# Performance work log

Hardware: AMD Instinct MI355X
Metric: run time of the kernel (lower is better)

## Reference

```python
import jax, jax.numpy as jnp
import numpy as np

N = 1_000_000
D1 = 16          # n_input_1 (first-layer features, cols 0:16)
D2 = 16          # n_input_2 (second-layer features, cols 16:32)
NC = 64          # n_clusters (first layer)
NCPC = 8         # n_clusters_per_cluster (second layer)


def setup_inputs() -> dict:
    key = jax.random.key(0)
    k1, k2, k3 = jax.random.split(key, 3)
    x = jax.random.normal(k1, (N, D1 + D2), dtype=jnp.float32)
    centers_outer = jax.random.normal(k2, (NC, D1), dtype=jnp.float32)
    centers_inner = jax.random.normal(k3, (NC, NCPC, D2), dtype=jnp.float32)
    return {"x": x, "centers_outer": centers_outer, "centers_inner": centers_inner}


def reference(x, centers_outer, centers_inner):
    # x: [N, D1+D2]; input_1_idx = cols [0:D1], input_2_idx = cols [D1:D1+D2]
    x1 = x[:, :D1]
    x2 = x[:, D1:]

    # First-layer nearest-centroid assignment (squared Euclidean).
    # ||x1 - c||^2 = ||x1||^2 - 2 x1.c + ||c||^2; the ||x1||^2 term is
    # constant over clusters so it does not affect the argmin.
    d1 = jnp.sum(centers_outer ** 2, axis=-1)[None, :] - 2.0 * (x1 @ centers_outer.T)  # [N, NC]
    outer = jnp.argmin(d1, axis=1)  # [N] int

    # Second-layer assignment: each sample only compares against the NCPC
    # sub-centers of its outer cluster (this fuses the original per-cluster
    # torch.where gather/scatter loop into one vectorized pass).
    sub = centers_inner[outer]  # [N, NCPC, D2] gather
    d2 = jnp.sum(sub ** 2, axis=-1) - 2.0 * jnp.einsum("nd,nkd->nk", x2, sub)  # [N, NCPC]
    inner = jnp.argmin(d2, axis=1)  # [N]

    return inner + outer * NCPC  # combined cluster id in [0, NC*NCPC)
```

## Files before the change

kernel.cpp:

```cpp
#include <hip/hip_runtime.h>

constexpr int D = 16;
constexpr int NC = 64;
constexpr int NCPC = 8;
constexpr int OSTRIDE = NCPC * D + 4;
constexpr int NPT = 2;
constexpr int BLOCK = 512;

__global__ __launch_bounds__(BLOCK, 2)
void cluster_kernel(const float* __restrict__ x,
                    const float* __restrict__ co,
                    const float* __restrict__ ci,
                    int* __restrict__ out, int n)
{
    __shared__ __align__(16) float s_ci[NC * OSTRIDE];
    __shared__ float s_inorm[NC * 9];

    const int t = threadIdx.x;

    const float4* ci4 = (const float4*)ci;
    #pragma unroll
    for (int i = 0; i < (NC * NCPC * D / 4) / BLOCK; ++i) {
        int idx = t + i * BLOCK;
        int o = idx >> 5;
        int f = idx & 31;
        float4 v = ci4[idx];
        *(float4*)&s_ci[o * OSTRIDE + f * 4] = v;
    }
    for (int i = t; i < NC * NCPC; i += BLOCK) {
        const float* src = ci + i * D;
        float s = 0.f;
        #pragma unroll
        for (int k = 0; k < D; ++k) s = fmaf(src[k], src[k], s);
        s_inorm[(i >> 3) * 9 + (i & 7)] = s;
    }
    float my_norm;
    {
        const float* c = co + (t & 63) * D;
        float s = 0.f;
        #pragma unroll
        for (int k = 0; k < D; ++k) s = fmaf(c[k], c[k], s);
        my_norm = s;
    }
    __syncthreads();

    const int base = blockIdx.x * (BLOCK * NPT) + t;
    #pragma unroll 1
    for (int it = 0; it < NPT; ++it) {
        int p = base + it * BLOCK;
        if (p < n) {
            const float4* xp = (const float4*)(x + (size_t)p * 32);
            float4 xa = xp[0], xb = xp[1], xc = xp[2], xd = xp[3];
            float x1[16] = {xa.x,xa.y,xa.z,xa.w, xb.x,xb.y,xb.z,xb.w,
                            xc.x,xc.y,xc.z,xc.w, xd.x,xd.y,xd.z,xd.w};

            float bestd = 3.4e38f;
            int bo = 0;
            #pragma unroll
            for (int j = 0; j < NC; ++j) {
                const float* c = co + j * D;
                float dot = 0.f;
                #pragma unroll
                for (int k = 0; k < D; ++k) dot = fmaf(x1[k], c[k], dot);
                float nj = __int_as_float(
                    __builtin_amdgcn_readlane(__float_as_int(my_norm), j));
                float d = fmaf(-2.f, dot, nj);
                if (d < bestd) { bestd = d; bo = j; }
            }

            float4 ya = xp[4], yb = xp[5], yc = xp[6], yd = xp[7];
            float x2[16] = {ya.x,ya.y,ya.z,ya.w, yb.x,yb.y,yb.z,yb.w,
                            yc.x,yc.y,yc.z,yc.w, yd.x,yd.y,yd.z,yd.w};

            const float* cb = s_ci + bo * OSTRIDE;
            const float* nb = s_inorm + bo * 9;
            float bestd2 = 3.4e38f;
            int bk = 0;
            #pragma unroll
            for (int k = 0; k < NCPC; ++k) {
                float4 c0 = *(const float4*)&cb[k * D + 0];
                float4 c1 = *(const float4*)&cb[k * D + 4];
                float4 c2 = *(const float4*)&cb[k * D + 8];
                float4 c3 = *(const float4*)&cb[k * D + 12];
                float dot = 0.f;
                dot = fmaf(x2[0],  c0.x, dot); dot = fmaf(x2[1],  c0.y, dot);
                dot = fmaf(x2[2],  c0.z, dot); dot = fmaf(x2[3],  c0.w, dot);
                dot = fmaf(x2[4],  c1.x, dot); dot = fmaf(x2[5],  c1.y, dot);
                dot = fmaf(x2[6],  c1.z, dot); dot = fmaf(x2[7],  c1.w, dot);
                dot = fmaf(x2[8],  c2.x, dot); dot = fmaf(x2[9],  c2.y, dot);
                dot = fmaf(x2[10], c2.z, dot); dot = fmaf(x2[11], c2.w, dot);
                dot = fmaf(x2[12], c3.x, dot); dot = fmaf(x2[13], c3.y, dot);
                dot = fmaf(x2[14], c3.z, dot); dot = fmaf(x2[15], c3.w, dot);
                float d = fmaf(-2.f, dot, nb[k]);
                if (d < bestd2) { bestd2 = d; bk = k; }
            }

            out[p] = bo * NCPC + bk;
        }
    }
}

extern "C" void kernel_launch(void* const* d_in, const int* in_sizes, int n_in,
                              void* d_out, int out_size, void* d_ws, size_t ws_size,
                              hipStream_t stream) {
    const float* x  = (const float*)d_in[0];
    const float* co = (const float*)d_in[1];
    const float* ci = (const float*)d_in[2];
    int* out = (int*)d_out;
    int n = in_sizes[0] / 32;
    int blocks = (n + BLOCK * NPT - 1) / (BLOCK * NPT);
    cluster_kernel<<<blocks, BLOCK, 0, stream>>>(x, co, ci, out, n);
}
```

Baseline: 198.0 us.

## Compute first-layer distances with bf16x3 split MFMA instead of scalar FMAs

The 64-centroid first-layer distance computation moves from per-thread scalar FMA loops to 32x32x16 bf16 MFMA instructions. Each fp32 operand is split into three bf16 pieces and six cross-product MFMAs are issued to keep near-fp32 accuracy. The centroid norms are folded into the accumulator init, and the argmin is reduced across the MFMA output layout and lane halves with a tie-break on the lower index. Block size and points per thread are retuned. The second-layer pass stays scalar. Rare argmin mismatches are possible from the extra rounding.

After: 191.9 us. 1.03x faster.

```diff
diff --git a/kernel.cpp b/kernel.cpp
--- a/kernel.cpp
+++ b/kernel.cpp
@@ -4,10 +4,22 @@
 constexpr int NC = 64;
 constexpr int NCPC = 8;
 constexpr int OSTRIDE = NCPC * D + 4;
-constexpr int NPT = 2;
-constexpr int BLOCK = 512;
+constexpr int BLOCK = 256;
+constexpr int NPT = 4;
 
-__global__ __launch_bounds__(BLOCK, 2)
+typedef __attribute__((ext_vector_type(8)))  short short8;
+typedef __attribute__((ext_vector_type(16))) float f32x16;
+
+static __device__ __forceinline__ unsigned f2bf(float f) {
+    unsigned u = __float_as_uint(f);
+    u += 0x7FFFu + ((u >> 16) & 1u);
+    return u >> 16;
+}
+static __device__ __forceinline__ float bf2f(unsigned h) {
+    return __uint_as_float(h << 16);
+}
+
+__global__ __launch_bounds__(BLOCK, 4)
 void cluster_kernel(const float* __restrict__ x,
                     const float* __restrict__ co,
                     const float* __restrict__ ci,
@@ -16,87 +28,160 @@
     __shared__ __align__(16) float s_ci[NC * OSTRIDE];
     __shared__ float s_inorm[NC * 9];
 
-    const int t = threadIdx.x;
+    const int t    = threadIdx.x;
+    const int lane = t & 63;
+    const int wave = t >> 6;
 
     const float4* ci4 = (const float4*)ci;
     #pragma unroll
-    for (int i = 0; i < (NC * NCPC * D / 4) / BLOCK; ++i) {
+    for (int i = 0; i < 8; ++i) {
         int idx = t + i * BLOCK;
-        int o = idx >> 5;
-        int f = idx & 31;
+        int o = idx >> 5, f = idx & 31;
         float4 v = ci4[idx];
         *(float4*)&s_ci[o * OSTRIDE + f * 4] = v;
     }
-    for (int i = t; i < NC * NCPC; i += BLOCK) {
+    #pragma unroll
+    for (int ii = 0; ii < 2; ++ii) {
+        int i = t + ii * BLOCK;
         const float* src = ci + i * D;
         float s = 0.f;
         #pragma unroll
         for (int k = 0; k < D; ++k) s = fmaf(src[k], src[k], s);
         s_inorm[(i >> 3) * 9 + (i & 7)] = s;
     }
+
     float my_norm;
     {
-        const float* c = co + (t & 63) * D;
+        const float* c = co + lane * D;
         float s = 0.f;
         #pragma unroll
         for (int k = 0; k < D; ++k) s = fmaf(c[k], c[k], s);
         my_norm = s;
     }
+
+    const int hi  = lane >> 5;
+    const int ks  = hi * 8;
+    const int hi4 = hi * 4;
+
+    float n_init[2][16];
+    #pragma unroll
+    for (int tc = 0; tc < 2; ++tc) {
+        #pragma unroll
+        for (int r = 0; r < 16; ++r) {
+            int c = tc * 32 + (r & 3) + 8 * (r >> 2) + hi4;
+            n_init[tc][r] = __int_as_float(
+                __builtin_amdgcn_ds_bpermute(c << 2, __float_as_int(my_norm)));
+        }
+    }
+
+    short8 a_h[2], a_m[2], a_l[2];
+    #pragma unroll
+    for (int tc = 0; tc < 2; ++tc) {
+        const float* cp = co + (tc * 32 + (lane & 31)) * D + ks;
+        float4 v0 = *(const float4*)cp;
+        float4 v1 = *(const float4*)(cp + 4);
+        float vv[8] = {v0.x,v0.y,v0.z,v0.w, v1.x,v1.y,v1.z,v1.w};
+        #pragma unroll
+        for (int j = 0; j < 8; ++j) {
+            float v = vv[j];
+            unsigned h = f2bf(v); float r1 = v - bf2f(h);
+            unsigned m = f2bf(r1); r1 = r1 - bf2f(m);
+            unsigned l2 = f2bf(r1);
+            a_h[tc][j] = (short)h; a_m[tc][j] = (short)m; a_l[tc][j] = (short)l2;
+        }
+    }
     __syncthreads();
 
-    const int base = blockIdx.x * (BLOCK * NPT) + t;
+    const int blockStart = blockIdx.x * (BLOCK * NPT);
     #pragma unroll 1
     for (int it = 0; it < NPT; ++it) {
-        int p = base + it * BLOCK;
-        if (p < n) {
-            const float4* xp = (const float4*)(x + (size_t)p * 32);
-            float4 xa = xp[0], xb = xp[1], xc = xp[2], xd = xp[3];
-            float x1[16] = {xa.x,xa.y,xa.z,xa.w, xb.x,xb.y,xb.z,xb.w,
-                            xc.x,xc.y,xc.z,xc.w, xd.x,xd.y,xd.z,xd.w};
+        const int S = blockStart + it * BLOCK + wave * 64;
 
-            float bestd = 3.4e38f;
-            int bo = 0;
+        int bo0 = 0, bo1 = 0;
+        #pragma unroll
+        for (int pt = 0; pt < 2; ++pt) {
+            int P = S + pt * 32 + (lane & 31);
+            P = P < n ? P : n - 1;
+            const float* xp = x + (size_t)P * 32 + ks;
+            float4 w0 = *(const float4*)xp;
+            float4 w1 = *(const float4*)(xp + 4);
+            float vv[8] = {w0.x,w0.y,w0.z,w0.w, w1.x,w1.y,w1.z,w1.w};
+            short8 b_h, b_m, b_l;
             #pragma unroll
-            for (int j = 0; j < NC; ++j) {
-                const float* c = co + j * D;
-                float dot = 0.f;
-                #pragma unroll
-                for (int k = 0; k < D; ++k) dot = fmaf(x1[k], c[k], dot);
-                float nj = __int_as_float(
-                    __builtin_amdgcn_readlane(__float_as_int(my_norm), j));
-                float d = fmaf(-2.f, dot, nj);
-                if (d < bestd) { bestd = d; bo = j; }
+            for (int j = 0; j < 8; ++j) {
+                float v = -2.0f * vv[j];
+                unsigned h = f2bf(v); float r1 = v - bf2f(h);
+                unsigned m = f2bf(r1); r1 = r1 - bf2f(m);
+                unsigned l2 = f2bf(r1);
+                b_h[j] = (short)h; b_m[j] = (short)m; b_l[j] = (short)l2;
             }
 
-            float4 ya = xp[4], yb = xp[5], yc = xp[6], yd = xp[7];
-            float x2[16] = {ya.x,ya.y,ya.z,ya.w, yb.x,yb.y,yb.z,yb.w,
-                            yc.x,yc.y,yc.z,yc.w, yd.x,yd.y,yd.z,yd.w};
+            f32x16 acc0, acc1;
+            #pragma unroll
+            for (int r = 0; r < 16; ++r) { acc0[r] = n_init[0][r]; acc1[r] = n_init[1][r]; }
+            acc0 = __builtin_amdgcn_mfma_f32_32x32x16_bf16(a_h[0], b_h, acc0, 0,0,0);
+            acc0 = __builtin_amdgcn_mfma_f32_32x32x16_bf16(a_h[0], b_m, acc0, 0,0,0);
+            acc0 = __builtin_amdgcn_mfma_f32_32x32x16_bf16(a_m[0], b_h, acc0, 0,0,0);
+            acc0 = __builtin_amdgcn_mfma_f32_32x32x16_bf16(a_h[0], b_l, acc0, 0,0,0);
+            acc0 = __builtin_amdgcn_mfma_f32_32x32x16_bf16(a_m[0], b_m, acc0, 0,0,0);
+            acc0 = __builtin_amdgcn_mfma_f32_32x32x16_bf16(a_l[0], b_h, acc0, 0,0,0);
+            acc1 = __builtin_amdgcn_mfma_f32_32x32x16_bf16(a_h[1], b_h, acc1, 0,0,0);
+            acc1 = __builtin_amdgcn_mfma_f32_32x32x16_bf16(a_h[1], b_m, acc1, 0,0,0);
+            acc1 = __builtin_amdgcn_mfma_f32_32x32x16_bf16(a_m[1], b_h, acc1, 0,0,0);
+            acc1 = __builtin_amdgcn_mfma_f32_32x32x16_bf16(a_h[1], b_l, acc1, 0,0,0);
+            acc1 = __builtin_amdgcn_mfma_f32_32x32x16_bf16(a_m[1], b_m, acc1, 0,0,0);
+            acc1 = __builtin_amdgcn_mfma_f32_32x32x16_bf16(a_l[1], b_h, acc1, 0,0,0);
 
-            const float* cb = s_ci + bo * OSTRIDE;
-            const float* nb = s_inorm + bo * 9;
-            float bestd2 = 3.4e38f;
-            int bk = 0;
+            float bestd = 3.4e38f; int bc = 0;
             #pragma unroll
-            for (int k = 0; k < NCPC; ++k) {
-                float4 c0 = *(const float4*)&cb[k * D + 0];
-                float4 c1 = *(const float4*)&cb[k * D + 4];
-                float4 c2 = *(const float4*)&cb[k * D + 8];
-                float4 c3 = *(const float4*)&cb[k * D + 12];
-                float dot = 0.f;
-                dot = fmaf(x2[0],  c0.x, dot); dot = fmaf(x2[1],  c0.y, dot);
-                dot = fmaf(x2[2],  c0.z, dot); dot = fmaf(x2[3],  c0.w, dot);
-                dot = fmaf(x2[4],  c1.x, dot); dot = fmaf(x2[5],  c1.y, dot);
-                dot = fmaf(x2[6],  c1.z, dot); dot = fmaf(x2[7],  c1.w, dot);
-                dot = fmaf(x2[8],  c2.x, dot); dot = fmaf(x2[9],  c2.y, dot);
-                dot = fmaf(x2[10], c2.z, dot); dot = fmaf(x2[11], c2.w, dot);
-                dot = fmaf(x2[12], c3.x, dot); dot = fmaf(x2[13], c3.y, dot);
-                dot = fmaf(x2[14], c3.z, dot); dot = fmaf(x2[15], c3.w, dot);
-                float d = fmaf(-2.f, dot, nb[k]);
-                if (d < bestd2) { bestd2 = d; bk = k; }
+            for (int tc = 0; tc < 2; ++tc) {
+                #pragma unroll
+                for (int r = 0; r < 16; ++r) {
+                    float d  = tc ? acc1[r] : acc0[r];
+                    int  cb = tc * 32 + (r & 3) + 8 * (r >> 2);
+                    if (d < bestd) { bestd = d; bc = cb; }
+                }
             }
+            int bestc = bc + hi4;
+            int pidx = (lane ^ 32) << 2;
+            float od = __int_as_float(
+                __builtin_amdgcn_ds_bpermute(pidx, __float_as_int(bestd)));
+            int   oc = __builtin_amdgcn_ds_bpermute(pidx, bestc);
+            if (od < bestd || (od == bestd && oc < bestc)) { bestd = od; bestc = oc; }
+            if (pt == 0) bo0 = bestc; else bo1 = bestc;
+        }
+        const int bo = (lane < 32) ? bo0 : bo1;
 
-            out[p] = bo * NCPC + bk;
+        const int p = S + lane;
+        const int q = p < n ? p : n - 1;
+        const float4* yp = (const float4*)(x + (size_t)q * 32 + 16);
+        float4 ya = yp[0], yb = yp[1], yc = yp[2], yd = yp[3];
+        float x2[16] = {ya.x,ya.y,ya.z,ya.w, yb.x,yb.y,yb.z,yb.w,
+                        yc.x,yc.y,yc.z,yc.w, yd.x,yd.y,yd.z,yd.w};
+        const float* cbp = s_ci + bo * OSTRIDE;
+        const float* nb  = s_inorm + bo * 9;
+        float bestd2 = 3.4e38f;
+        int bk = 0;
+        #pragma unroll
+        for (int k = 0; k < NCPC; ++k) {
+            float4 e0 = *(const float4*)&cbp[k * D + 0];
+            float4 e1 = *(const float4*)&cbp[k * D + 4];
+            float4 e2 = *(const float4*)&cbp[k * D + 8];
+            float4 e3 = *(const float4*)&cbp[k * D + 12];
+            float dot = 0.f;
+            dot = fmaf(x2[0],  e0.x, dot); dot = fmaf(x2[1],  e0.y, dot);
+            dot = fmaf(x2[2],  e0.z, dot); dot = fmaf(x2[3],  e0.w, dot);
+            dot = fmaf(x2[4],  e1.x, dot); dot = fmaf(x2[5],  e1.y, dot);
+            dot = fmaf(x2[6],  e1.z, dot); dot = fmaf(x2[7],  e1.w, dot);
+            dot = fmaf(x2[8],  e2.x, dot); dot = fmaf(x2[9],  e2.y, dot);
+            dot = fmaf(x2[10], e2.z, dot); dot = fmaf(x2[11], e2.w, dot);
+            dot = fmaf(x2[12], e3.x, dot); dot = fmaf(x2[13], e3.y, dot);
+            dot = fmaf(x2[14], e3.z, dot); dot = fmaf(x2[15], e3.w, dot);
+            float d2v = fmaf(-2.f, dot, nb[k]);
+            if (d2v < bestd2) { bestd2 = d2v; bk = k; }
         }
+
+        if (p < n) out[p] = bo * NCPC + bk;
     }
 }
 
```
